# Kernel optimization log

Measured on AMD Instinct MI355X. Metric: run time of the kernel, lower is better.

Reference implementation:

```python
import jax, jax.numpy as jnp
import numpy as np

L = 3        # num_decoder_layers
H = 1024     # num_decoder_hidden (also input_size and embed dim)
V = 100      # num_decoder_tokens (start_symbol = V, embedding has V+1 rows)
O = 1024     # num_joiner_hidden
B = 64       # batch size
U_MAX = 256  # y sequence length; loop runs U_MAX+1 steps


def setup_inputs() -> dict:
    key = jax.random.key(0)
    ks = jax.random.split(key, 10)
    s = 1.0 / np.sqrt(H)  # torch GRUCell init bound
    return {
        "y": jax.random.randint(ks[0], (B, U_MAX), 0, V),
        "U": jax.random.randint(ks[9], (B,), 1, U_MAX + 1),
        "embed": jax.random.normal(ks[1], (V + 1, H), dtype=jnp.float32),
        "W_ih": jax.random.uniform(ks[2], (L, 3 * H, H), minval=-s, maxval=s, dtype=jnp.float32),
        "W_hh": jax.random.uniform(ks[3], (L, 3 * H, H), minval=-s, maxval=s, dtype=jnp.float32),
        "b_ih": jax.random.uniform(ks[4], (L, 3 * H), minval=-s, maxval=s, dtype=jnp.float32),
        "b_hh": jax.random.uniform(ks[5], (L, 3 * H), minval=-s, maxval=s, dtype=jnp.float32),
        "init_state": jax.random.normal(ks[6], (L, H), dtype=jnp.float32),
        "lin_W": jax.random.uniform(ks[7], (O, H), minval=-s, maxval=s, dtype=jnp.float32),
        "lin_b": jax.random.uniform(ks[8], (O,), minval=-s, maxval=s, dtype=jnp.float32),
    }


def gru_cell(x, h, Wih, Whh, bih, bhh):
    # torch.nn.GRUCell math
    gi = x @ Wih.T + bih          # [B, 3H]
    gh = h @ Whh.T + bhh          # [B, 3H]
    i_r, i_z, i_n = jnp.split(gi, 3, axis=-1)
    h_r, h_z, h_n = jnp.split(gh, 3, axis=-1)
    r = jax.nn.sigmoid(i_r + h_r)
    z = jax.nn.sigmoid(i_z + h_z)
    n = jnp.tanh(i_n + r * h_n)
    return (1.0 - z) * n + z * h


def reference(y, U, embed, W_ih, W_hh, b_ih, b_hh, init_state, lin_W, lin_b):
    # U is unused by the original forward's math (only y.shape[1] matters).
    del U
    bsz = y.shape[0]
    start = embed.shape[0] - 1  # start_symbol = num_decoder_tokens
    # tokens at step u: start symbol at u=0, then y[:, u-1]  -> [B, U_max+1]
    tokens = jnp.concatenate([jnp.full((bsz, 1), start, dtype=y.dtype), y], axis=1)
    state0 = jnp.broadcast_to(init_state, (bsz,) + init_state.shape)  # [B, L, H]

    n_layers = W_ih.shape[0]

    def step(state, tok):
        x = embed[tok]  # [B, H]
        new_states = []
        for l in range(n_layers):  # small fixed layer loop
            x = gru_cell(x, state[:, l], W_ih[l], W_hh[l], b_ih[l], b_hh[l])
            new_states.append(x)
            # dropout p=0.5 is identity in eval mode
        state = jnp.stack(new_states, axis=1)  # [B, L, H]
        out = state[:, -1] @ lin_W.T + lin_b   # [B, O]
        return state, out

    _, outs = jax.lax.scan(step, state0, tokens.T)  # outs: [U_max+1, B, O]
    return jnp.transpose(outs, (1, 0, 2))           # [B, U_max+1, O]
```

## Files before the change

kernel.cpp:

```cpp
#include <hip/hip_runtime.h>
#include <hip/hip_cooperative_groups.h>
#include <stdint.h>

namespace cg = cooperative_groups;

typedef unsigned short u16;
typedef unsigned long long u64;
typedef __bf16 b8v __attribute__((ext_vector_type(8)));
typedef float  f4v __attribute__((ext_vector_type(4)));

#define NB      256
#define NSTAGE  260

#define WS_HB16   0UL
#define WS_INIT16 786432UL
#define WS_EMB16  792576UL
#define WS_PWG    1048576UL
#define WS_PWP    38797312UL
#define WS_ARR    40894464UL
#define WS_GCT    40898560UL
#define WS_REL    40898816UL
#define WS_NEED   40902912UL

#define N_GRU_GRP  2359296
#define N_PRJ_GRP  131072
#define N_EMB_GRP  12928
#define N_TOT_GRP  2503680

__device__ __forceinline__ float sigm(float x) { return 1.0f / (1.0f + __expf(-x)); }
__device__ __forceinline__ float tanh_f(float x) {
  float ax = fabsf(x);
  float e = __expf(-2.0f * ax);
  float m = (1.0f - e) / (1.0f + e);
  return x >= 0.0f ? m : -m;
}
__device__ __forceinline__ u16 f2b(float f) {
  union { float f; uint32_t u; } x; x.f = f;
  uint32_t r = x.u + 0x7fffu + ((x.u >> 16) & 1u);
  return (u16)(r >> 16);
}
__device__ __forceinline__ b8v cvt8(f4v lo, f4v hi) {
  b8v v;
  v[0] = (__bf16)lo[0]; v[1] = (__bf16)lo[1]; v[2] = (__bf16)lo[2]; v[3] = (__bf16)lo[3];
  v[4] = (__bf16)hi[0]; v[5] = (__bf16)hi[1]; v[6] = (__bf16)hi[2]; v[7] = (__bf16)hi[3];
  return v;
}

__device__ __forceinline__ b8v gload16(const u16* p) {
  b8v v;
  asm volatile("global_load_dwordx4 %0, %1, off sc0 sc1"
               : "=&v"(v) : "v"(p));
  return v;
}
__device__ __forceinline__ void astore8(u16* p, u16 a, u16 b, u16 c, u16 d) {
  union { u16 s[4]; u64 q; } u;
  u.s[0] = a; u.s[1] = b; u.s[2] = c; u.s[3] = d;
  __hip_atomic_store((u64*)p, u.q, __ATOMIC_RELAXED, __HIP_MEMORY_SCOPE_AGENT);
}
__device__ __forceinline__ int ld_i(const int* p) {
  return __hip_atomic_load(p, __ATOMIC_RELAXED, __HIP_MEMORY_SCOPE_AGENT);
}
__device__ __forceinline__ void st_i(int* p, int v) {
  __hip_atomic_store(p, v, __ATOMIC_RELAXED, __HIP_MEMORY_SCOPE_AGENT);
}

template<int R, int WN>
__device__ __forceinline__ void gru_round(
    b8v (&fa)[4][2][4], const u16* const (&rowp)[4],
    const b8v (&wreg)[3][4][4], f4v (&acc)[3][4])
{
  asm volatile("s_waitcnt vmcnt(%0)" :: "n"(WN));
  __builtin_amdgcn_sched_barrier(0);
  #pragma unroll
  for (int g = 0; g < 3; ++g)
    #pragma unroll
    for (int tti = 0; tti < 2; ++tti)
      #pragma unroll
      for (int mi = 0; mi < 4; ++mi)
        acc[g][mi] = __builtin_amdgcn_mfma_f32_16x16x32_bf16(
            fa[R & 3][tti][mi], wreg[g][R >> 1][(R & 1) * 2 + tti],
            acc[g][mi], 0, 0, 0);
  if (R < 4) {
    #pragma unroll
    for (int tti = 0; tti < 2; ++tti)
      #pragma unroll
      for (int mi = 0; mi < 4; ++mi)
        fa[R & 3][tti][mi] = gload16(rowp[mi] + (R + 4) * 64 + tti * 32);
  }
}

template<int R, int WN>
__device__ __forceinline__ void prj_round(
    b8v (&fr)[4][2][4], const b8v (&wreg)[3][4][4], f4v (&acc)[4])
{
  asm volatile("s_waitcnt vmcnt(%0)" :: "n"(WN));
  __builtin_amdgcn_sched_barrier(0);
  #pragma unroll
  for (int tti = 0; tti < 2; ++tti)
    #pragma unroll
    for (int mi = 0; mi < 4; ++mi)
      acc[mi] = __builtin_amdgcn_mfma_f32_16x16x32_bf16(
          fr[R][tti][mi], wreg[0][R >> 1][(R & 1) * 2 + tti],
          acc[mi], 0, 0, 0);
}

__global__ __launch_bounds__(256) void prep(
    const float* __restrict__ embed, const float* __restrict__ Wih,
    const float* __restrict__ Whh, const float* __restrict__ initS,
    const float* __restrict__ linW, unsigned char* __restrict__ ws)
{
  int idx = blockIdx.x * 256 + threadIdx.x;
  if (idx < 33) *(int*)(ws + WS_ARR + (size_t)idx * 256) = 0;
  if (idx < N_GRU_GRP) {
    int sid = idx >> 11, w = idx & 2047;
    int q = sid % 6, lct = sid / 6;
    int ct = lct & 63, l = lct >> 6;
    int s = w >> 8, tt = (w >> 6) & 3, lane = w & 63;
    int gate = q >> 1, p = q & 1;
    int row = gate * 1024 + ct * 16 + (lane & 15);
    int k0  = s * 128 + tt * 32 + (lane >> 4) * 8;
    const float* src = (p ? Whh : Wih) + (size_t)l * 3145728 + (size_t)row * 1024 + k0;
    *(b8v*)(ws + WS_PWG + (size_t)idx * 16) =
        cvt8(*(const f4v*)src, *(const f4v*)(src + 4));
  } else if (idx < N_GRU_GRP + N_PRJ_GRP) {
    int i2 = idx - N_GRU_GRP;
    int ct = i2 >> 11, w = i2 & 2047;
    int s = w >> 8, tt = (w >> 6) & 3, lane = w & 63;
    int row = ct * 16 + (lane & 15);
    int k0  = s * 128 + tt * 32 + (lane >> 4) * 8;
    const float* src = linW + (size_t)row * 1024 + k0;
    *(b8v*)(ws + WS_PWP + (size_t)i2 * 16) =
        cvt8(*(const f4v*)src, *(const f4v*)(src + 4));
  } else if (idx < N_GRU_GRP + N_PRJ_GRP + N_EMB_GRP) {
    int i3 = idx - (N_GRU_GRP + N_PRJ_GRP);
    const float* src = embed + (size_t)i3 * 8;
    *(b8v*)(ws + WS_EMB16 + (size_t)i3 * 16) =
        cvt8(*(const f4v*)src, *(const f4v*)(src + 4));
  } else if (idx < N_TOT_GRP) {
    int i4 = idx - (N_GRU_GRP + N_PRJ_GRP + N_EMB_GRP);
    const float* src = initS + (size_t)i4 * 8;
    *(b8v*)(ws + WS_INIT16 + (size_t)i4 * 16) =
        cvt8(*(const f4v*)src, *(const f4v*)(src + 4));
  }
}

__global__ __launch_bounds__(256, 1) void dec_fast(
    const int* __restrict__ y,
    const float* __restrict__ bih, const float* __restrict__ bhh,
    const float* __restrict__ initS, const float* __restrict__ linb,
    float* __restrict__ out, unsigned char* __restrict__ ws)
{
  __shared__ __align__(16) float gate_lds[12][64][20];

  const int tid  = threadIdx.x;
  const int bid  = blockIdx.x;
  const int l    = bid >> 6;
  const int ct   = bid & 63;
  const int c0   = ct << 4;
  const int wv   = tid >> 6;
  const int lane = tid & 63;
  const int lq   = lane >> 4;
  const int ln   = lane & 15;
  const int part = wv & 1;
  const int kh   = wv >> 1;

  u16* hb16        = (u16*)(ws + WS_HB16);
  const u16* ini16 = (const u16*)(ws + WS_INIT16);
  const u16* emb16 = (const u16*)(ws + WS_EMB16);

  int* const myarr = (int*)(ws + WS_ARR + (size_t)(bid & 15) * 256);
  int* const gctr  = (int*)(ws + WS_GCT);
  int* const myrel = (int*)(ws + WS_REL + (size_t)(bid & 15) * 256);
  unsigned char* const relb = ws + WS_REL;

  b8v wreg[3][4][4];
  if (l < 3) {
    const unsigned char* wst = ws + WS_PWG + (size_t)(l * 64 + ct) * 196608;
    #pragma unroll
    for (int g = 0; g < 3; ++g)
      #pragma unroll
      for (int si = 0; si < 4; ++si)
        #pragma unroll
        for (int tt = 0; tt < 4; ++tt)
          wreg[g][si][tt] = *(const b8v*)(wst + (size_t)(g * 2 + part) * 32768
                                              + (size_t)(kh * 4 + si) * 4096
                                              + (size_t)tt * 1024 + (size_t)lane * 16);
  } else {
    const unsigned char* wst = ws + WS_PWP + (size_t)ct * 32768;
    #pragma unroll
    for (int si = 0; si < 2; ++si)
      #pragma unroll
      for (int tt = 0; tt < 4; ++tt)
        wreg[0][si][tt] = *(const b8v*)(wst + (size_t)(wv * 2 + si) * 4096
                                            + (size_t)tt * 1024 + (size_t)lane * 16);
  }

  const int eb = tid >> 2;
  const int cc = (tid & 3) << 2;
  const int cg = c0 + cc;
  float hold[4];
  float rb[4], zb[4], ib[4], hbv[4];
  if (l < 3) {
    const float* biL = bih + l * 3072;
    const float* bhL = bhh + l * 3072;
    #pragma unroll
    for (int j = 0; j < 4; ++j) {
      hold[j] = initS[(l << 10) + cg + j];
      rb[j]  = biL[cg + j]        + bhL[cg + j];
      zb[j]  = biL[1024 + cg + j] + bhL[1024 + cg + j];
      ib[j]  = biL[2048 + cg + j];
      hbv[j] = bhL[2048 + cg + j];
    }
  }
  f4v pbias = (f4v){0.f, 0.f, 0.f, 0.f};
  if (l == 3) pbias = *(const f4v*)(linb + cg);

  int tokCur[4] = {100, 100, 100, 100};

  for (int t = 0; t < NSTAGE; ++t) {
    const int u = t - l;
    const bool active = (u >= 0) && (u <= 256);
    const int rp = (t + 1) & 1;
    const int wp = t & 1;
    if (active) {
      if (l < 3) {
        const int koff0 = (kh << 9) + (lq << 3);
        const u16* rowp[4];
        if (part == 0) {
          if (l == 0) {
            #pragma unroll
            for (int mi = 0; mi < 4; ++mi)
              rowp[mi] = emb16 + ((size_t)tokCur[mi] << 10) + koff0;
          } else {
            const u16* xb = hb16 + (((l - 1) * 2 + rp) << 16) + koff0;
            #pragma unroll
            for (int mi = 0; mi < 4; ++mi)
              rowp[mi] = xb + ((mi * 16 + ln) << 10);
          }
        } else {
          if (u == 0) {
            const u16* hb = ini16 + (l << 10) + koff0;
            #pragma unroll
            for (int mi = 0; mi < 4; ++mi) rowp[mi] = hb;
          } else {
            const u16* hb = hb16 + ((l * 2 + rp) << 16) + koff0;
            #pragma unroll
            for (int mi = 0; mi < 4; ++mi)
              rowp[mi] = hb + ((mi * 16 + ln) << 10);
          }
        }

        int tokNext[4];
        const bool wantTok = (l == 0) && (part == 0) && (u < 256);
        if (wantTok) {
          #pragma unroll
          for (int mi = 0; mi < 4; ++mi)
            tokNext[mi] = y[((mi * 16 + ln) << 8) + u];
        }
        __builtin_amdgcn_sched_barrier(0);

        f4v acc[3][4];
        #pragma unroll
        for (int g = 0; g < 3; ++g)
          #pragma unroll
          for (int mi = 0; mi < 4; ++mi)
            acc[g][mi] = (f4v){0.f, 0.f, 0.f, 0.f};

        b8v fa[4][2][4];
        #pragma unroll
        for (int rr = 0; rr < 4; ++rr)
          #pragma unroll
          for (int tti = 0; tti < 2; ++tti)
            #pragma unroll
            for (int mi = 0; mi < 4; ++mi)
              fa[rr][tti][mi] = gload16(rowp[mi] + rr * 64 + tti * 32);

        gru_round<0, 24>(fa, rowp, wreg, acc);
        gru_round<1, 24>(fa, rowp, wreg, acc);
        gru_round<2, 24>(fa, rowp, wreg, acc);
        gru_round<3, 24>(fa, rowp, wreg, acc);
        gru_round<4, 24>(fa, rowp, wreg, acc);
        gru_round<5, 16>(fa, rowp, wreg, acc);
        gru_round<6, 8>(fa, rowp, wreg, acc);
        gru_round<7, 0>(fa, rowp, wreg, acc);

        #pragma unroll
        for (int g = 0; g < 3; ++g)
          #pragma unroll
          for (int mi = 0; mi < 4; ++mi)
            #pragma unroll
            for (int r4 = 0; r4 < 4; ++r4)
              gate_lds[wv * 3 + g][mi * 16 + lq * 4 + r4][ln] = acc[g][mi][r4];
        __syncthreads();

        {
          const f4v v0  = *(const f4v*)&gate_lds[0][eb][cc];
          const f4v v1  = *(const f4v*)&gate_lds[1][eb][cc];
          const f4v v2  = *(const f4v*)&gate_lds[2][eb][cc];
          const f4v v3  = *(const f4v*)&gate_lds[3][eb][cc];
          const f4v v4  = *(const f4v*)&gate_lds[4][eb][cc];
          const f4v v5  = *(const f4v*)&gate_lds[5][eb][cc];
          const f4v v6  = *(const f4v*)&gate_lds[6][eb][cc];
          const f4v v7  = *(const f4v*)&gate_lds[7][eb][cc];
          const f4v v8  = *(const f4v*)&gate_lds[8][eb][cc];
          const f4v v9  = *(const f4v*)&gate_lds[9][eb][cc];
          const f4v v10 = *(const f4v*)&gate_lds[10][eb][cc];
          const f4v v11 = *(const f4v*)&gate_lds[11][eb][cc];
          u16 pk[4];
          #pragma unroll
          for (int j = 0; j < 4; ++j) {
            float rg = sigm(v0[j] + v6[j] + v3[j] + v9[j] + rb[j]);
            float zg = sigm(v1[j] + v7[j] + v4[j] + v10[j] + zb[j]);
            float ng = tanh_f(v2[j] + v8[j] + ib[j] + rg * (v5[j] + v11[j] + hbv[j]));
            float hn = (1.0f - zg) * ng + zg * hold[j];
            hold[j] = hn;
            pk[j] = f2b(hn);
          }
          astore8(hb16 + ((l * 2 + wp) << 16) + (eb << 10) + cg,
                  pk[0], pk[1], pk[2], pk[3]);
        }
        if (wantTok) {
          #pragma unroll
          for (int mi = 0; mi < 4; ++mi) tokCur[mi] = tokNext[mi];
        }
      } else {
        const u16* xb = hb16 + ((4 + rp) << 16) + (wv << 8) + (lq << 3);
        const u16* rowp[4];
        #pragma unroll
        for (int mi = 0; mi < 4; ++mi) rowp[mi] = xb + ((mi * 16 + ln) << 10);

        f4v acc[4];
        #pragma unroll
        for (int mi = 0; mi < 4; ++mi) acc[mi] = (f4v){0.f, 0.f, 0.f, 0.f};

        b8v fr[4][2][4];
        #pragma unroll
        for (int rr = 0; rr < 4; ++rr)
          #pragma unroll
          for (int tti = 0; tti < 2; ++tti)
            #pragma unroll
            for (int mi = 0; mi < 4; ++mi)
              fr[rr][tti][mi] = gload16(rowp[mi] + rr * 64 + tti * 32);

        prj_round<0, 24>(fr, wreg, acc);
        prj_round<1, 16>(fr, wreg, acc);
        prj_round<2, 8>(fr, wreg, acc);
        prj_round<3, 0>(fr, wreg, acc);

        #pragma unroll
        for (int mi = 0; mi < 4; ++mi)
          #pragma unroll
          for (int r4 = 0; r4 < 4; ++r4)
            gate_lds[wv][mi * 16 + lq * 4 + r4][ln] = acc[mi][r4];
        __syncthreads();

        {
          const f4v s0 = *(const f4v*)&gate_lds[0][eb][cc];
          const f4v s1 = *(const f4v*)&gate_lds[1][eb][cc];
          const f4v s2 = *(const f4v*)&gate_lds[2][eb][cc];
          const f4v s3 = *(const f4v*)&gate_lds[3][eb][cc];
          f4v v = s0 + s1 + s2 + s3 + pbias;
          *(f4v*)(out + (((size_t)(eb * 257 + u)) << 10) + cg) = v;
        }
      }
    }

    if (t + 1 < NSTAGE) {
      __syncthreads();
      if (tid == 0) {
        const int tgt = t + 1;
        int old = __hip_atomic_fetch_add(myarr, 1, __ATOMIC_RELAXED,
                                         __HIP_MEMORY_SCOPE_AGENT);
        if (old + 1 == (tgt << 4)) {
          int gold = __hip_atomic_fetch_add(gctr, 1, __ATOMIC_RELAXED,
                                            __HIP_MEMORY_SCOPE_AGENT);
          if (gold + 1 == (tgt << 4)) {
            #pragma unroll
            for (int r = 0; r < 16; ++r)
              st_i((int*)(relb + (size_t)r * 256), tgt);
          }
        }
        while (ld_i(myrel) < tgt) __builtin_amdgcn_s_sleep(1);
      }
      __syncthreads();
    }
  }
}

__global__ __launch_bounds__(256) void dec_slow(
    const int* __restrict__ y, const float* __restrict__ embed,
    const float* __restrict__ Wih, const float* __restrict__ Whh,
    const float* __restrict__ bih, const float* __restrict__ bhh,
    const float* __restrict__ initS, const float* __restrict__ linW,
    const float* __restrict__ linb, float* __restrict__ out,
    unsigned char* __restrict__ ws)
{
  cg::grid_group grid = cg::this_grid();
  __shared__ b8v a_lds[2048];
  __shared__ float gate_lds[4][64][17];
  __shared__ int tok_lds[64];
  const int tid = threadIdx.x, bid = blockIdx.x;
  const int l = bid >> 6, c0 = (bid & 63) << 4;
  const int wv = tid >> 6, lane = tid & 63, lq = lane >> 4, ln = lane & 15;
  float* hb32 = (float*)ws;
  const int rowoff = (wv == 0) ? c0 : (wv == 1) ? (1024 + c0) : (2048 + c0);
  const size_t wl = (size_t)(l < 3 ? l : 0) * 3072 * 1024;
  const float* WihL = Wih + wl;
  const float* WhhL = Whh + wl;
  for (int t = 0; t < NSTAGE; ++t) {
    const int u = t - l;
    const bool active = (u >= 0) && (u <= 256);
    const int rp = (t + 1) & 1, wp = t & 1;
    if (active) {
      if (l == 0 && tid < 64)
        tok_lds[tid] = (u == 0) ? 100 : y[(tid << 8) + (u - 1)];
      if (l < 3) {
        f4v acc[4];
        #pragma unroll
        for (int mi = 0; mi < 4; ++mi) acc[mi] = (f4v){0.f, 0.f, 0.f, 0.f};
        const float* xbase = (l == 0) ? embed : (hb32 + (((l - 1) * 2 + rp) << 16));
        const float* hbase = hb32 + ((l * 2 + rp) << 16);
        for (int s = 0; s < 8; ++s) {
          __syncthreads();
          #pragma unroll
          for (int i = 0; i < 8; ++i) {
            int g = tid + (i << 8);
            int sec = g >> 10, gg = g & 1023, b = gg & 63, k8 = gg >> 6;
            int koff = (s << 7) + (k8 << 3);
            const float* src;
            if (sec == 0) src = (l == 0) ? embed + ((size_t)tok_lds[b] << 10) + koff
                                         : xbase + (b << 10) + koff;
            else src = (u == 0) ? initS + (l << 10) + koff : hbase + (b << 10) + koff;
            a_lds[((sec << 4) + k8) * 64 + b] = cvt8(*(const f4v*)src, *(const f4v*)(src + 4));
          }
          __syncthreads();
          const int pstart = (wv == 3) ? 1 : 0;
          const int pend = (wv == 2) ? 1 : 2;
          for (int part = pstart; part < pend; ++part) {
            const float* wrow = ((part == 0) ? WihL : WhhL)
                              + (size_t)(rowoff + ln) * 1024 + (s << 7) + (lq << 3);
            #pragma unroll
            for (int tt = 0; tt < 4; ++tt) {
              b8v bf = cvt8(*(const f4v*)(wrow + (tt << 5)), *(const f4v*)(wrow + (tt << 5) + 4));
              int fb = ((part << 4) + (tt << 2) + lq) * 64 + ln;
              #pragma unroll
              for (int mi = 0; mi < 4; ++mi)
                acc[mi] = __builtin_amdgcn_mfma_f32_16x16x32_bf16(a_lds[fb + (mi << 4)], bf, acc[mi], 0, 0, 0);
            }
          }
        }
        #pragma unroll
        for (int mi = 0; mi < 4; ++mi)
          #pragma unroll
          for (int r = 0; r < 4; ++r)
            gate_lds[wv][(mi << 4) + (lq << 2) + r][ln] = acc[mi][r];
        __syncthreads();
        {
          const int b = tid >> 2, cc = (tid & 3) << 2, cg = c0 + cc;
          const float* biL = bih + l * 3072;
          const float* bhL = bhh + l * 3072;
          float hold[4];
          if (u == 0) {
            #pragma unroll
            for (int j = 0; j < 4; ++j) hold[j] = initS[(l << 10) + cg + j];
          } else {
            const float* hp = hb32 + ((size_t)(l * 2 + rp) << 16) + (b << 10) + cg;
            #pragma unroll
            for (int j = 0; j < 4; ++j) hold[j] = hp[j];
          }
          float* o32 = hb32 + ((size_t)(l * 2 + wp) << 16) + (b << 10) + cg;
          #pragma unroll
          for (int j = 0; j < 4; ++j) {
            int c = cg + j;
            float rpre = gate_lds[0][b][cc + j] + biL[c] + bhL[c];
            float zpre = gate_lds[1][b][cc + j] + biL[1024 + c] + bhL[1024 + c];
            float inn = gate_lds[2][b][cc + j] + biL[2048 + c];
            float hnn = gate_lds[3][b][cc + j] + bhL[2048 + c];
            float rg = sigm(rpre), zg = sigm(zpre);
            float ng = tanh_f(inn + rg * hnn);
            o32[j] = (1.0f - zg) * ng + zg * hold[j];
          }
        }
      } else {
        f4v acc1 = (f4v){0.f, 0.f, 0.f, 0.f};
        const float* xbase = hb32 + ((4 + rp) << 16);
        for (int s = 0; s < 8; ++s) {
          __syncthreads();
          #pragma unroll
          for (int i = 0; i < 4; ++i) {
            int g = tid + (i << 8);
            int b = g & 63, k8 = g >> 6;
            const float* src = xbase + (b << 10) + (s << 7) + (k8 << 3);
            a_lds[k8 * 64 + b] = cvt8(*(const f4v*)src, *(const f4v*)(src + 4));
          }
          __syncthreads();
          const float* wrow = linW + (size_t)(c0 + ln) * 1024 + (s << 7) + (lq << 3);
          #pragma unroll
          for (int tt = 0; tt < 4; ++tt) {
            b8v bf = cvt8(*(const f4v*)(wrow + (tt << 5)), *(const f4v*)(wrow + (tt << 5) + 4));
            acc1 = __builtin_amdgcn_mfma_f32_16x16x32_bf16(
                     a_lds[((tt << 2) + lq) * 64 + (wv << 4) + ln], bf, acc1, 0, 0, 0);
          }
        }
        const float bias = linb[c0 + ln];
        #pragma unroll
        for (int r = 0; r < 4; ++r) {
          int b = (wv << 4) + (lq << 2) + r;
          out[((size_t)(b * 257 + u) << 10) + c0 + ln] = acc1[r] + bias;
        }
      }
    }
    grid.sync();
  }
}

extern "C" void kernel_launch(void* const* d_in, const int* in_sizes, int n_in,
                              void* d_out, int out_size, void* d_ws, size_t ws_size,
                              hipStream_t stream) {
  const int* y        = (const int*)d_in[0];
  const float* embed  = (const float*)d_in[2];
  const float* Wih    = (const float*)d_in[3];
  const float* Whh    = (const float*)d_in[4];
  const float* bih    = (const float*)d_in[5];
  const float* bhh    = (const float*)d_in[6];
  const float* initS  = (const float*)d_in[7];
  const float* linW   = (const float*)d_in[8];
  const float* linb   = (const float*)d_in[9];
  float* out = (float*)d_out;
  unsigned char* ws = (unsigned char*)d_ws;

  if (ws_size >= WS_NEED) {
    hipLaunchKernelGGL(prep, dim3(N_TOT_GRP / 256), dim3(256), 0, stream,
                       embed, Wih, Whh, initS, linW, ws);
    hipLaunchKernelGGL(dec_fast, dim3(NB), dim3(256), 0, stream,
                       y, bih, bhh, initS, linb, out, ws);
  } else {
    void* args[] = {(void*)&y, (void*)&embed, (void*)&Wih, (void*)&Whh,
                    (void*)&bih, (void*)&bhh, (void*)&initS, (void*)&linW,
                    (void*)&linb, (void*)&out, (void*)&ws};
    hipLaunchCooperativeKernel((void*)dec_slow, dim3(NB), dim3(256), args, 0, stream);
  }
}
```

Baseline: 2.818 ms.

## Replace atomic-counter grid barrier with per-block flag slots polled by block zero

The two-level atomic fetch-add grid barrier is replaced by per-block arrival flags. Each block stores its step number into its own slot, and one wavefront of block 0 polls all 256 slots in parallel with a wave-wide vote. Block 0 then writes the 16 release flags that the other blocks spin on. This removes serialized atomic contention on shared counters, but the release now depends on the polling latency of a single block.

```diff
diff --git a/kernel.cpp b/kernel.cpp
--- a/kernel.cpp
+++ b/kernel.cpp
@@ -17,10 +17,9 @@
 #define WS_EMB16  792576UL
 #define WS_PWG    1048576UL
 #define WS_PWP    38797312UL
-#define WS_ARR    40894464UL
-#define WS_GCT    40898560UL
-#define WS_REL    40898816UL
-#define WS_NEED   40902912UL
+#define WS_SLOT   40894464UL
+#define WS_REL    40960000UL
+#define WS_NEED   40964096UL
 
 #define N_GRU_GRP  2359296
 #define N_PRJ_GRP  131072
@@ -110,7 +109,7 @@
     const float* __restrict__ linW, unsigned char* __restrict__ ws)
 {
   int idx = blockIdx.x * 256 + threadIdx.x;
-  if (idx < 33) *(int*)(ws + WS_ARR + (size_t)idx * 256) = 0;
+  if (idx < 272) *(int*)(ws + WS_SLOT + (size_t)idx * 256) = 0;
   if (idx < N_GRU_GRP) {
     int sid = idx >> 11, w = idx & 2047;
     int q = sid % 6, lct = sid / 6;
@@ -168,10 +167,10 @@
   const u16* ini16 = (const u16*)(ws + WS_INIT16);
   const u16* emb16 = (const u16*)(ws + WS_EMB16);
 
-  int* const myarr = (int*)(ws + WS_ARR + (size_t)(bid & 15) * 256);
-  int* const gctr  = (int*)(ws + WS_GCT);
-  int* const myrel = (int*)(ws + WS_REL + (size_t)(bid & 15) * 256);
-  unsigned char* const relb = ws + WS_REL;
+  int* const myslot = (int*)(ws + WS_SLOT + (size_t)bid * 256);
+  int* const myrel  = (int*)(ws + WS_REL + (size_t)(bid & 15) * 256);
+  const int* const pollbase =
+      (const int*)(ws + WS_SLOT + (size_t)lane * 1024);
 
   b8v wreg[3][4][4];
   if (l < 3) {
@@ -367,20 +366,27 @@
 
     if (t + 1 < NSTAGE) {
       __syncthreads();
-      if (tid == 0) {
-        const int tgt = t + 1;
-        int old = __hip_atomic_fetch_add(myarr, 1, __ATOMIC_RELAXED,
-                                         __HIP_MEMORY_SCOPE_AGENT);
-        if (old + 1 == (tgt << 4)) {
-          int gold = __hip_atomic_fetch_add(gctr, 1, __ATOMIC_RELAXED,
-                                            __HIP_MEMORY_SCOPE_AGENT);
-          if (gold + 1 == (tgt << 4)) {
-            #pragma unroll
-            for (int r = 0; r < 16; ++r)
-              st_i((int*)(relb + (size_t)r * 256), tgt);
-          }
-        }
-        while (ld_i(myrel) < tgt) __builtin_amdgcn_s_sleep(1);
+      const int tgt = t + 1;
+      if (bid == 0) {
+        if (tid < 64) {
+          if (tid == 0) st_i(myslot, tgt);
+          for (;;) {
+            int a0 = ld_i(pollbase);
+            int a1 = ld_i((const int*)((const unsigned char*)pollbase + 256));
+            int a2 = ld_i((const int*)((const unsigned char*)pollbase + 512));
+            int a3 = ld_i((const int*)((const unsigned char*)pollbase + 768));
+            bool ok = (a0 >= tgt) & (a1 >= tgt) & (a2 >= tgt) & (a3 >= tgt);
+            if (__all(ok)) break;
+            __builtin_amdgcn_s_sleep(1);
+          }
+          if (tid < 16)
+            st_i((int*)(ws + WS_REL + (size_t)tid * 256), tgt);
+        }
+      } else {
+        if (tid == 0) {
+          st_i(myslot, tgt);
+          while (ld_i(myrel) < tgt) __builtin_amdgcn_s_sleep(1);
+        }
       }
       __syncthreads();
     }
```

After: 2.896 ms. 1.03x slower.
